# Kernel tuning notes

Hardware: AMD Instinct MI355X
Metric: run time of the kernel (lower is better)

The kernel has to match this reference:

```python
import jax, jax.numpy as jnp
import numpy as np

VOCAB = 50257
HIDDEN = 1024
CUTOFFS = [0, 20000, 40000, VOCAB]
N_CLUSTERS = 3
N_TOKENS = 4096


def setup_inputs() -> dict:
    key = jax.random.key(0)
    k1, k2, k3, k4 = jax.random.split(key, 4)
    x = jax.random.normal(k1, (N_TOKENS, HIDDEN), dtype=jnp.float32)
    y = jax.random.randint(k2, (N_TOKENS,), 0, VOCAB, dtype=jnp.int64)
    # nn.Linear(hidden, n_clusters, bias=False) weight: [n_clusters, hidden], init std=0.02
    W_cluster = jax.random.normal(k3, (N_CLUSTERS, HIDDEN), dtype=jnp.float32) * 0.02
    logits = jax.random.normal(k4, (HIDDEN, VOCAB), dtype=jnp.float32) * 0.02
    return {"x": x, "y": y, "W_cluster": W_cluster, "logits": logits}


def reference(x, y, W_cluster, logits):
    # cluster head: [N, n_clusters]
    cluster_ll = jax.nn.log_softmax(x @ W_cluster.T, axis=1)
    nll = jnp.zeros(y.shape, dtype=x.dtype)
    for i in range(N_CLUSTERS):  # small fixed loop over clusters
        l, r = CUTOFFS[i], CUTOFFS[i + 1]
        mask = (y >= l) & (y < r)
        # tail logits for this cluster's vocab slice: [N, r-l]
        tail_logprob = jax.nn.log_softmax(x @ logits[:, l:r], axis=1)
        t = jnp.clip(y - l, 0, r - l - 1)  # in-range for masked-out tokens
        tgt_lp = jnp.take_along_axis(tail_logprob, t[:, None], axis=1)[:, 0]
        val = -cluster_ll[:, i] - tgt_lp
        nll = jnp.where(mask, val, nll)
    return nll
```

## Files before the change

### kernel.cpp

```cpp
#include <hip/hip_runtime.h>
#include <math.h>

typedef unsigned short ushort_t;
typedef __attribute__((ext_vector_type(8))) short short8;
typedef __attribute__((ext_vector_type(4))) float floatx4;

constexpr int NT = 4096;
constexpr int H  = 1024;
constexpr int V  = 50257;
constexpr int CUT1 = 20000;
constexpr int CUT2 = 40000;

constexpr int NPAD_TOK = 4224;
constexpr int NPAD_COL = 50432;
constexpr int CT0 = 157, CT1 = 157, CT2 = 81;
constexpr int CT_TOTAL = CT0 + CT1 + CT2;
constexpr int MAX_TTILES = 32;
constexpr int CT_GROUPS = (CT_TOTAL + 7) / 8;
constexpr int MFMA_GRID = 8 * CT_GROUPS * MAX_TTILES;

constexpr int FB_TILES0 = (20000 + 63) / 64;
constexpr int FB_TILES1 = (20000 + 63) / 64;
constexpr int FB_TILES2 = (V - 40000 + 63) / 64;
constexpr int FB_TOTAL = FB_TILES0 + FB_TILES1 + FB_TILES2;

__device__ __forceinline__ ushort_t f2bf(float f) {
  unsigned int u = __float_as_uint(f);
  u = (u + 0x7FFFu + ((u >> 16) & 1u)) >> 16;
  return (ushort_t)u;
}
__device__ __forceinline__ float bf2f(ushort_t b) {
  return __uint_as_float(((unsigned int)b) << 16);
}
__device__ __forceinline__ void gl_lds16(const void* g, void* l) {
  __builtin_amdgcn_global_load_lds(
      (const __attribute__((address_space(1))) void*)g,
      (__attribute__((address_space(3))) void*)l, 16, 0, 0);
}

__global__ __launch_bounds__(1024) void setup_kernel(
    const int* __restrict__ y, int* __restrict__ offsets,
    int* __restrict__ perm, float* __restrict__ sumexp) {
  __shared__ int wcnt[16][3];
  __shared__ int wstart[16][3];
  int tid = threadIdx.x, lane = tid & 63, wid = tid >> 6;
  for (int i = tid; i < NT; i += 1024) sumexp[i] = 0.f;

  int kc[4];
  unsigned long long msk[4][3];
  int cw0 = 0, cw1 = 0, cw2 = 0;
  #pragma unroll
  for (int e = 0; e < 4; e++) {
    int v = y[tid + e * 1024];
    kc[e] = (v >= CUT1) + (v >= CUT2);
    msk[e][0] = __ballot(kc[e] == 0);
    msk[e][1] = __ballot(kc[e] == 1);
    msk[e][2] = __ballot(kc[e] == 2);
    cw0 += __popcll(msk[e][0]);
    cw1 += __popcll(msk[e][1]);
    cw2 += __popcll(msk[e][2]);
  }
  if (lane == 0) { wcnt[wid][0] = cw0; wcnt[wid][1] = cw1; wcnt[wid][2] = cw2; }
  __syncthreads();
  if (tid == 0) {
    int t0 = 0, t1 = 0, t2 = 0;
    for (int wv = 0; wv < 16; wv++) { t0 += wcnt[wv][0]; t1 += wcnt[wv][1]; t2 += wcnt[wv][2]; }
    offsets[0] = 0; offsets[1] = t0; offsets[2] = t0 + t1; offsets[3] = NT;
    int c0 = 0, c1 = t0, c2 = t0 + t1;
    for (int wv = 0; wv < 16; wv++) {
      wstart[wv][0] = c0; c0 += wcnt[wv][0];
      wstart[wv][1] = c1; c1 += wcnt[wv][1];
      wstart[wv][2] = c2; c2 += wcnt[wv][2];
    }
  }
  __syncthreads();
  int r0 = wstart[wid][0], r1 = wstart[wid][1], r2 = wstart[wid][2];
  unsigned long long below = (1ull << lane) - 1ull;
  #pragma unroll
  for (int e = 0; e < 4; e++) {
    int t = tid + e * 1024;
    int c = kc[e];
    int start = (c == 0) ? r0 : ((c == 1) ? r1 : r2);
    perm[start + __popcll(msk[e][c] & below)] = t;
    r0 += __popcll(msk[e][0]);
    r1 += __popcll(msk[e][1]);
    r2 += __popcll(msk[e][2]);
  }
}

__global__ __launch_bounds__(256) void gather_kernel(
    const float* __restrict__ x, const int* __restrict__ perm,
    ushort_t* __restrict__ xb) {
  int p = blockIdx.x;
  int src = (p < NT) ? perm[p] : -1;
  int k = threadIdx.x * 4;
  ushort4 o;
  if (src >= 0) {
    float4 v = *(const float4*)&x[(size_t)src * H + k];
    o.x = f2bf(v.x); o.y = f2bf(v.y); o.z = f2bf(v.z); o.w = f2bf(v.w);
  } else {
    o.x = 0; o.y = 0; o.z = 0; o.w = 0;
  }
  *(ushort4*)&xb[(size_t)p * H + k] = o;
}

__global__ __launch_bounds__(256) void transpose_kernel(
    const float* __restrict__ logits, ushort_t* __restrict__ lt) {
  __shared__ float ts[64][129];
  int col0 = blockIdx.x * 128, k0 = blockIdx.y * 64;
  int tid = threadIdx.x;
  #pragma unroll
  for (int e = 0; e < 8; e++) {
    int i = e * 256 + tid;
    int r = i >> 5, q = i & 31;
    int col = col0 + q * 4;
    float4 v;
    if (col + 3 < V) {
      v = *(const float4*)&logits[(size_t)(k0 + r) * V + col];
    } else {
      v.x = (col + 0 < V) ? logits[(size_t)(k0 + r) * V + col + 0] : 0.f;
      v.y = (col + 1 < V) ? logits[(size_t)(k0 + r) * V + col + 1] : 0.f;
      v.z = (col + 2 < V) ? logits[(size_t)(k0 + r) * V + col + 2] : 0.f;
      v.w = (col + 3 < V) ? logits[(size_t)(k0 + r) * V + col + 3] : 0.f;
    }
    ts[r][4 * q + 0] = v.x;
    ts[r][4 * q + 1] = v.y;
    ts[r][4 * q + 2] = v.z;
    ts[r][4 * q + 3] = v.w;
  }
  __syncthreads();
  #pragma unroll
  for (int e = 0; e < 4; e++) {
    int i = e * 256 + tid;
    int col = i >> 3, kq8 = i & 7;
    short8 o;
    #pragma unroll
    for (int d = 0; d < 8; d++) o[d] = (short)f2bf(ts[8 * kq8 + d][col]);
    *(short8*)&lt[(size_t)(col0 + col) * H + k0 + 8 * kq8] = o;
  }
}

__global__ __launch_bounds__(256) void head_kernel(
    const float* __restrict__ x, const int* __restrict__ y,
    const float* __restrict__ Wc, const ushort_t* __restrict__ lt,
    float* __restrict__ neg_cll, float* __restrict__ z_tgt) {
  int tid = threadIdx.x;
  int lane = tid & 63;
  int token = blockIdx.x * 4 + (tid >> 6);
  int yv = y[token];
  const float* xp = x + (size_t)token * H;
  const ushort_t* lp = lt + (size_t)yv * H;
  float c0 = 0.f, c1 = 0.f, c2 = 0.f, zt = 0.f;
  #pragma unroll
  for (int j = 0; j < 16; j++) {
    int h = lane + j * 64;
    float xv = xp[h];
    c0 = fmaf(xv, Wc[h], c0);
    c1 = fmaf(xv, Wc[H + h], c1);
    c2 = fmaf(xv, Wc[2 * H + h], c2);
    zt = fmaf(xv, bf2f(lp[h]), zt);
  }
  #pragma unroll
  for (int d = 32; d; d >>= 1) {
    c0 += __shfl_down(c0, d);
    c1 += __shfl_down(c1, d);
    c2 += __shfl_down(c2, d);
    zt += __shfl_down(zt, d);
  }
  if (lane == 0) {
    float m = fmaxf(c0, fmaxf(c1, c2));
    float lse = m + logf(expf(c0 - m) + expf(c1 - m) + expf(c2 - m));
    int k = (yv >= CUT1) + (yv >= CUT2);
    float ck = (k == 0) ? c0 : ((k == 1) ? c1 : c2);
    neg_cll[token] = lse - ck;
    z_tgt[token] = zt;
  }
}

__global__ __launch_bounds__(256) void mfma_kernel(
    const ushort_t* __restrict__ xb, const ushort_t* __restrict__ lt,
    const int* __restrict__ offsets, float* __restrict__ sumexp) {
  int id = blockIdx.x;
  int xcd = id & 7;
  int j = id >> 3;
  int ct = xcd + 8 * (j >> 5);
  int tt = j & 31;
  if (ct >= CT_TOTAL) return;

  int c, col0, colEnd;
  if (ct < CT0)            { c = 0; col0 = ct * 128;                      colEnd = CUT1; }
  else if (ct < CT0 + CT1) { c = 1; col0 = CUT1 + (ct - CT0) * 128;       colEnd = CUT2; }
  else                     { c = 2; col0 = CUT2 + (ct - CT0 - CT1) * 128; colEnd = V; }

  int t0 = offsets[c] + tt * 128;
  int tEnd = offsets[c + 1];
  if (t0 >= tEnd) return;

  __shared__ __align__(16) ushort_t xs[2][128 * 64];
  __shared__ __align__(16) ushort_t ls[2][128 * 64];

  int tid = threadIdx.x;
  int lane = tid & 63;
  int w = tid >> 6;
  int wm = w >> 1, wn = w & 1;
  int m_in = lane & 15, quad = lane >> 4;

  int srow = lane >> 3;
  int sc = lane & 7;
  int gchunk = sc ^ srow;
  const ushort_t* ga[4];
  const ushort_t* gb[4];
  int lofs[4];
  #pragma unroll
  for (int cc = 0; cc < 4; cc++) {
    int r0 = w * 32 + cc * 8;
    ga[cc] = xb + (size_t)(t0 + r0 + srow) * H + gchunk * 8;
    gb[cc] = lt + (size_t)(col0 + r0 + srow) * H + gchunk * 8;
    lofs[cc] = r0 * 64;
  }

  floatx4 acc[4][4];
  #pragma unroll
  for (int i = 0; i < 4; i++)
    #pragma unroll
    for (int jj = 0; jj < 4; jj++)
      acc[i][jj] = (floatx4){0.f, 0.f, 0.f, 0.f};

  auto STAGE = [&](int b) {
    #pragma unroll
    for (int cc = 0; cc < 4; cc++) {
      gl_lds16(ga[cc], &xs[b][lofs[cc]]);
      gl_lds16(gb[cc], &ls[b][lofs[cc]]);
      ga[cc] += 64; gb[cc] += 64;
    }
  };

  auto COMPUTE = [&](int b) {
    #pragma unroll
    for (int h = 0; h < 2; h++) {
      short8 af[4], bf[4];
      #pragma unroll
      for (int i = 0; i < 4; i++) {
        int row = wm * 64 + i * 16 + m_in;
        int slot = (h * 4 + quad) ^ (row & 7);
        af[i] = *(const short8*)&xs[b][row * 64 + slot * 8];
      }
      #pragma unroll
      for (int jj = 0; jj < 4; jj++) {
        int row = wn * 64 + jj * 16 + m_in;
        int slot = (h * 4 + quad) ^ (row & 7);
        bf[jj] = *(const short8*)&ls[b][row * 64 + slot * 8];
      }
      __builtin_amdgcn_s_setprio(1);
      #pragma unroll
      for (int i = 0; i < 4; i++)
        #pragma unroll
        for (int jj = 0; jj < 4; jj++)
          acc[i][jj] = __builtin_amdgcn_mfma_f32_16x16x32_bf16(af[i], bf[jj], acc[i][jj], 0, 0, 0);
      __builtin_amdgcn_s_setprio(0);
    }
  };

  STAGE(0);
  int cur = 0;
  #pragma unroll
  for (int t = 0; t < 15; ++t) {
    STAGE(cur ^ 1);
    asm volatile("s_waitcnt vmcnt(8)" ::: "memory");
    __builtin_amdgcn_sched_barrier(0);
    __builtin_amdgcn_s_barrier();
    __builtin_amdgcn_sched_barrier(0);
    COMPUTE(cur);
    __builtin_amdgcn_sched_barrier(0);
    __builtin_amdgcn_s_barrier();
    __builtin_amdgcn_sched_barrier(0);
    cur ^= 1;
  }
  asm volatile("s_waitcnt vmcnt(0)" ::: "memory");
  __builtin_amdgcn_sched_barrier(0);
  __builtin_amdgcn_s_barrier();
  __builtin_amdgcn_sched_barrier(0);
  COMPUTE(cur);

  __syncthreads();
  float* red = (float*)&xs[0][0];
  #pragma unroll
  for (int i = 0; i < 4; i++) {
    #pragma unroll
    for (int r = 0; r < 4; r++) {
      float s = 0.f;
      #pragma unroll
      for (int jj = 0; jj < 4; jj++) {
        int col = col0 + wn * 64 + jj * 16 + m_in;
        if (col < colEnd) s += __expf(acc[i][jj][r]);
      }
      s += __shfl_down(s, 8, 16);
      s += __shfl_down(s, 4, 16);
      s += __shfl_down(s, 2, 16);
      s += __shfl_down(s, 1, 16);
      if (m_in == 0) red[w * 64 + i * 16 + quad * 4 + r] = s;
    }
  }
  __syncthreads();
  if (tid < 128) {
    int rl = tid & 63, wm2 = tid >> 6;
    float s = red[(wm2 * 2 + 0) * 64 + rl] + red[(wm2 * 2 + 1) * 64 + rl];
    if (t0 + tid < tEnd) atomicAdd(&sumexp[t0 + tid], s);
  }
}

__global__ __launch_bounds__(256) void final_kernel(
    const int* __restrict__ perm, const float* __restrict__ neg_cll,
    const float* __restrict__ z_tgt, const float* __restrict__ sumexp,
    float* __restrict__ out) {
  int p = blockIdx.x * 256 + threadIdx.x;
  if (p < NT) {
    int t = perm[p];
    out[t] = neg_cll[t] + logf(sumexp[p]) - z_tgt[t];
  }
}

__global__ __launch_bounds__(256) void head_kernel_fb(
    const float* __restrict__ x, const int* __restrict__ y,
    const float* __restrict__ Wc, const float* __restrict__ logits,
    float* __restrict__ neg_cll, float* __restrict__ z_tgt) {
  int tid = threadIdx.x;
  int lane = tid & 63;
  int token = blockIdx.x * 4 + (tid >> 6);
  int yv = y[token];
  const float* xp = x + (size_t)token * H;
  float c0 = 0.f, c1 = 0.f, c2 = 0.f, zt = 0.f;
  #pragma unroll
  for (int j = 0; j < 16; j++) {
    int h = lane + j * 64;
    float xv = xp[h];
    c0 = fmaf(xv, Wc[h], c0);
    c1 = fmaf(xv, Wc[H + h], c1);
    c2 = fmaf(xv, Wc[2 * H + h], c2);
    zt = fmaf(xv, logits[(size_t)h * V + yv], zt);
  }
  #pragma unroll
  for (int d = 32; d; d >>= 1) {
    c0 += __shfl_down(c0, d);
    c1 += __shfl_down(c1, d);
    c2 += __shfl_down(c2, d);
    zt += __shfl_down(zt, d);
  }
  if (lane == 0) {
    float m = fmaxf(c0, fmaxf(c1, c2));
    float lse = m + logf(expf(c0 - m) + expf(c1 - m) + expf(c2 - m));
    int k = (yv >= CUT1) + (yv >= CUT2);
    float ck = (k == 0) ? c0 : ((k == 1) ? c1 : c2);
    neg_cll[token] = lse - ck;
    z_tgt[token] = zt;
  }
}

__global__ __launch_bounds__(256) void main_kernel_fb(
    const float* __restrict__ x, const float* __restrict__ logits,
    const int* __restrict__ offsets, const int* __restrict__ perm,
    float* __restrict__ sumexp) {
  int ct = blockIdx.x;
  int c, lct;
  if (ct < FB_TILES0)                  { c = 0; lct = ct; }
  else if (ct < FB_TILES0 + FB_TILES1) { c = 1; lct = ct - FB_TILES0; }
  else                                 { c = 2; lct = ct - FB_TILES0 - FB_TILES1; }
  int colBase = (c == 0) ? 0 : ((c == 1) ? CUT1 : CUT2);
  int colEnd  = (c == 0) ? CUT1 : ((c == 1) ? CUT2 : V);
  int col0 = colBase + lct * 64;
  int ncols = min(64, colEnd - col0);

  int t0 = offsets[c] + blockIdx.y * 64;
  int tEnd = offsets[c + 1];
  if (t0 >= tEnd) return;
  int ntok = min(64, tEnd - t0);

  __shared__ int tok_s[64];
  __shared__ float xsf[32][68];
  __shared__ float lsm[32][68];

  int tid = threadIdx.x;
  if (tid < 64) tok_s[tid] = perm[t0 + min(tid, ntok - 1)];
  __syncthreads();

  int tg = tid >> 4;
  int cg = tid & 15;
  float acc[4][4] = {};

  for (int h0 = 0; h0 < H; h0 += 32) {
    __syncthreads();
    #pragma unroll
    for (int e = 0; e < 8; e++) {
      int elem = e * 256 + tid;
      int tt = elem >> 5, kk = elem & 31;
      xsf[kk][tt] = x[(size_t)tok_s[tt] * H + h0 + kk];
    }
    #pragma unroll
    for (int e = 0; e < 8; e++) {
      int elem = e * 256 + tid;
      int kk = elem >> 6, cc = elem & 63;
      lsm[kk][cc] = (cc < ncols) ? logits[(size_t)(h0 + kk) * V + col0 + cc] : 0.f;
    }
    __syncthreads();
    #pragma unroll
    for (int kk = 0; kk < 32; kk++) {
      float4 xv = *(const float4*)&xsf[kk][4 * tg];
      float4 lv = *(const float4*)&lsm[kk][4 * cg];
      acc[0][0] = fmaf(xv.x, lv.x, acc[0][0]);
      acc[0][1] = fmaf(xv.x, lv.y, acc[0][1]);
      acc[0][2] = fmaf(xv.x, lv.z, acc[0][2]);
      acc[0][3] = fmaf(xv.x, lv.w, acc[0][3]);
      acc[1][0] = fmaf(xv.y, lv.x, acc[1][0]);
      acc[1][1] = fmaf(xv.y, lv.y, acc[1][1]);
      acc[1][2] = fmaf(xv.y, lv.z, acc[1][2]);
      acc[1][3] = fmaf(xv.y, lv.w, acc[1][3]);
      acc[2][0] = fmaf(xv.z, lv.x, acc[2][0]);
      acc[2][1] = fmaf(xv.z, lv.y, acc[2][1]);
      acc[2][2] = fmaf(xv.z, lv.z, acc[2][2]);
      acc[2][3] = fmaf(xv.z, lv.w, acc[2][3]);
      acc[3][0] = fmaf(xv.w, lv.x, acc[3][0]);
      acc[3][1] = fmaf(xv.w, lv.y, acc[3][1]);
      acc[3][2] = fmaf(xv.w, lv.z, acc[3][2]);
      acc[3][3] = fmaf(xv.w, lv.w, acc[3][3]);
    }
  }

  float s[4];
  #pragma unroll
  for (int i = 0; i < 4; i++) {
    float v = 0.f;
    #pragma unroll
    for (int j = 0; j < 4; j++) {
      if (4 * cg + j < ncols) v += expf(acc[i][j]);
    }
    s[i] = v;
  }
  #pragma unroll
  for (int i = 0; i < 4; i++) {
    #pragma unroll
    for (int d = 8; d; d >>= 1) s[i] += __shfl_down(s[i], d, 16);
  }
  if (cg == 0) {
    #pragma unroll
    for (int i = 0; i < 4; i++) {
      int tt = 4 * tg + i;
      if (tt < ntok) atomicAdd(&sumexp[tok_s[tt]], s[i]);
    }
  }
}

__global__ __launch_bounds__(256) void final_kernel_fb(
    const float* __restrict__ neg_cll, const float* __restrict__ z_tgt,
    const float* __restrict__ sumexp, float* __restrict__ out) {
  int i = blockIdx.x * 256 + threadIdx.x;
  if (i < NT) out[i] = neg_cll[i] + logf(sumexp[i]) - z_tgt[i];
}

extern "C" void kernel_launch(void* const* d_in, const int* in_sizes, int n_in,
                              void* d_out, int out_size, void* d_ws,
                              size_t ws_size, hipStream_t stream) {
  const float* x      = (const float*)d_in[0];
  const int*   y      = (const int*)d_in[1];
  const float* Wc     = (const float*)d_in[2];
  const float* logits = (const float*)d_in[3];
  float* out = (float*)d_out;

  char* ws = (char*)d_ws;
  int*   offsets = (int*)ws;
  int*   perm    = (int*)(ws + 256);
  float* sumexp  = (float*)(ws + 16896);
  float* neg_cll = (float*)(ws + 33280);
  float* z_tgt   = (float*)(ws + 49664);
  ushort_t* xb   = (ushort_t*)(ws + 66048);
  ushort_t* lt   = (ushort_t*)(ws + 66048 + (size_t)NPAD_TOK * H * 2);
  const size_t WS_NEED = 66048 + (size_t)NPAD_TOK * H * 2 + (size_t)NPAD_COL * H * 2;

  setup_kernel<<<1, 1024, 0, stream>>>(y, offsets, perm, sumexp);

  if (ws_size >= WS_NEED) {
    gather_kernel<<<NPAD_TOK, 256, 0, stream>>>(x, perm, xb);
    dim3 tg(NPAD_COL / 128, H / 64);
    transpose_kernel<<<tg, 256, 0, stream>>>(logits, lt);
    head_kernel<<<NT / 4, 256, 0, stream>>>(x, y, Wc, lt, neg_cll, z_tgt);
    mfma_kernel<<<MFMA_GRID, 256, 0, stream>>>(xb, lt, offsets, sumexp);
    final_kernel<<<NT / 256, 256, 0, stream>>>(perm, neg_cll, z_tgt, sumexp, out);
  } else {
    head_kernel_fb<<<NT / 4, 256, 0, stream>>>(x, y, Wc, logits, neg_cll, z_tgt);
    dim3 grid(FB_TOTAL, 64);
    main_kernel_fb<<<grid, 256, 0, stream>>>(x, logits, offsets, perm, sumexp);
    final_kernel_fb<<<NT / 256, 256, 0, stream>>>(neg_cll, z_tgt, sumexp, out);
  }
}
```

Before: 560.9 us.

## Enlarge MFMA GEMM tiles to 256x256 with 8 waves and 4-stage K pipeline

The fused GEMM+sumexp kernel moves from 128x128 output tiles with 4 waves and a 2-stage, K=64 double buffer to 256x256 tiles with 8 waves (each computing 128x64) and a 4-deep ring of K=32 slices with a new swizzled LDS layout. Larger tiles double the operand reuse per loaded byte and cut the number of global loads, atomics and blocks. A deeper prefetch hides latency with one barrier per K step. The cost is more register pressure (32 accumulators per wave), more padding waste on the cluster boundaries, and fewer blocks to fill the GPU.

Measured after the change: 582.8 us. 1.04x slower.

```diff
diff --git a/kernel.cpp b/kernel.cpp
--- a/kernel.cpp
+++ b/kernel.cpp
@@ -11,13 +11,14 @@
 constexpr int CUT1 = 20000;
 constexpr int CUT2 = 40000;
 
-constexpr int NPAD_TOK = 4224;
-constexpr int NPAD_COL = 50432;
-constexpr int CT0 = 157, CT1 = 157, CT2 = 81;
+constexpr int NPAD_TOK = 4352;
+constexpr int NPAD_COL = 50560;
+constexpr int CT0 = 79, CT1 = 79, CT2 = 41;
 constexpr int CT_TOTAL = CT0 + CT1 + CT2;
-constexpr int MAX_TTILES = 32;
+constexpr int MAX_TTILES = 16;
 constexpr int CT_GROUPS = (CT_TOTAL + 7) / 8;
 constexpr int MFMA_GRID = 8 * CT_GROUPS * MAX_TTILES;
+constexpr int NKT = H / 32;
 
 constexpr int FB_TILES0 = (20000 + 63) / 64;
 constexpr int FB_TILES1 = (20000 + 63) / 64;
@@ -177,115 +178,125 @@
   }
 }
 
-__global__ __launch_bounds__(256) void mfma_kernel(
+__global__ __launch_bounds__(512, 2) void mfma_kernel(
     const ushort_t* __restrict__ xb, const ushort_t* __restrict__ lt,
     const int* __restrict__ offsets, float* __restrict__ sumexp) {
   int id = blockIdx.x;
   int xcd = id & 7;
   int j = id >> 3;
-  int ct = xcd + 8 * (j >> 5);
-  int tt = j & 31;
+  int ct = xcd + 8 * (j >> 4);
+  int tt = j & 15;
   if (ct >= CT_TOTAL) return;
 
   int c, col0, colEnd;
-  if (ct < CT0)            { c = 0; col0 = ct * 128;                      colEnd = CUT1; }
-  else if (ct < CT0 + CT1) { c = 1; col0 = CUT1 + (ct - CT0) * 128;       colEnd = CUT2; }
-  else                     { c = 2; col0 = CUT2 + (ct - CT0 - CT1) * 128; colEnd = V; }
-
-  int t0 = offsets[c] + tt * 128;
+  if (ct < CT0)            { c = 0; col0 = ct * 256;                      colEnd = CUT1; }
+  else if (ct < CT0 + CT1) { c = 1; col0 = CUT1 + (ct - CT0) * 256;       colEnd = CUT2; }
+  else                     { c = 2; col0 = CUT2 + (ct - CT0 - CT1) * 256; colEnd = V; }
+
+  int t0 = offsets[c] + tt * 256;
   int tEnd = offsets[c + 1];
   if (t0 >= tEnd) return;
 
-  __shared__ __align__(16) ushort_t xs[2][128 * 64];
-  __shared__ __align__(16) ushort_t ls[2][128 * 64];
+  __shared__ __align__(16) ushort_t As[4][128 * 64];
+  __shared__ __align__(16) ushort_t Bs[4][128 * 64];
 
   int tid = threadIdx.x;
   int lane = tid & 63;
   int w = tid >> 6;
-  int wm = w >> 1, wn = w & 1;
+  int wm = w >> 2, wn = w & 3;
   int m_in = lane & 15, quad = lane >> 4;
 
-  int srow = lane >> 3;
-  int sc = lane & 7;
-  int gchunk = sc ^ srow;
-  const ushort_t* ga[4];
-  const ushort_t* gb[4];
-  int lofs[4];
-  #pragma unroll
-  for (int cc = 0; cc < 4; cc++) {
-    int r0 = w * 32 + cc * 8;
-    ga[cc] = xb + (size_t)(t0 + r0 + srow) * H + gchunk * 8;
-    gb[cc] = lt + (size_t)(col0 + r0 + srow) * H + gchunk * 8;
-    lofs[cc] = r0 * 64;
-  }
-
-  floatx4 acc[4][4];
-  #pragma unroll
-  for (int i = 0; i < 4; i++)
+  const ushort_t* gA[2];
+  const ushort_t* gB[2];
+  #pragma unroll
+  for (int cc = 0; cc < 2; cc++) {
+    int lr = w * 16 + cc * 8 + (lane >> 3);
+    int ls = lane & 7;
+    int m  = 2 * lr + (ls >> 2);
+    int q  = (ls & 3) ^ (lr & 3);
+    gA[cc] = xb + (size_t)(t0 + m) * H + q * 8;
+    gB[cc] = lt + (size_t)(col0 + m) * H + q * 8;
+  }
+  int ks = 0;
+  auto STAGE = [&]() {
+    int b = ks & 3;
+    #pragma unroll
+    for (int cc = 0; cc < 2; cc++) {
+      gl_lds16(gA[cc], &As[b][(w * 16 + cc * 8) * 64]);
+      gl_lds16(gB[cc], &Bs[b][(w * 16 + cc * 8) * 64]);
+      gA[cc] += 32; gB[cc] += 32;
+    }
+    ++ks;
+  };
+
+  int sxor = quad ^ ((m_in >> 1) & 3);
+  int aoff = (wm * 64 + (m_in >> 1)) * 64 + (m_in & 1) * 32 + sxor * 8;
+  int boff = (wn * 32 + (m_in >> 1)) * 64 + (m_in & 1) * 32 + sxor * 8;
+
+  floatx4 acc[8][4];
+  #pragma unroll
+  for (int i = 0; i < 8; i++)
     #pragma unroll
     for (int jj = 0; jj < 4; jj++)
       acc[i][jj] = (floatx4){0.f, 0.f, 0.f, 0.f};
 
-  auto STAGE = [&](int b) {
-    #pragma unroll
-    for (int cc = 0; cc < 4; cc++) {
-      gl_lds16(ga[cc], &xs[b][lofs[cc]]);
-      gl_lds16(gb[cc], &ls[b][lofs[cc]]);
-      ga[cc] += 64; gb[cc] += 64;
-    }
-  };
-
-  auto COMPUTE = [&](int b) {
-    #pragma unroll
-    for (int h = 0; h < 2; h++) {
-      short8 af[4], bf[4];
-      #pragma unroll
-      for (int i = 0; i < 4; i++) {
-        int row = wm * 64 + i * 16 + m_in;
-        int slot = (h * 4 + quad) ^ (row & 7);
-        af[i] = *(const short8*)&xs[b][row * 64 + slot * 8];
-      }
-      #pragma unroll
-      for (int jj = 0; jj < 4; jj++) {
-        int row = wn * 64 + jj * 16 + m_in;
-        int slot = (h * 4 + quad) ^ (row & 7);
-        bf[jj] = *(const short8*)&ls[b][row * 64 + slot * 8];
-      }
-      __builtin_amdgcn_s_setprio(1);
-      #pragma unroll
-      for (int i = 0; i < 4; i++)
-        #pragma unroll
-        for (int jj = 0; jj < 4; jj++)
-          acc[i][jj] = __builtin_amdgcn_mfma_f32_16x16x32_bf16(af[i], bf[jj], acc[i][jj], 0, 0, 0);
-      __builtin_amdgcn_s_setprio(0);
-    }
-  };
-
-  STAGE(0);
-  int cur = 0;
-  #pragma unroll
-  for (int t = 0; t < 15; ++t) {
-    STAGE(cur ^ 1);
-    asm volatile("s_waitcnt vmcnt(8)" ::: "memory");
-    __builtin_amdgcn_sched_barrier(0);
-    __builtin_amdgcn_s_barrier();
-    __builtin_amdgcn_sched_barrier(0);
-    COMPUTE(cur);
-    __builtin_amdgcn_sched_barrier(0);
-    __builtin_amdgcn_s_barrier();
-    __builtin_amdgcn_sched_barrier(0);
-    cur ^= 1;
-  }
-  asm volatile("s_waitcnt vmcnt(0)" ::: "memory");
+  STAGE(); STAGE(); STAGE();
+  asm volatile("s_waitcnt vmcnt(8)" ::: "memory");
   __builtin_amdgcn_sched_barrier(0);
   __builtin_amdgcn_s_barrier();
   __builtin_amdgcn_sched_barrier(0);
-  COMPUTE(cur);
-
-  __syncthreads();
-  float* red = (float*)&xs[0][0];
-  #pragma unroll
-  for (int i = 0; i < 4; i++) {
+
+  #pragma unroll 4
+  for (int k = 0; k < NKT; ++k) {
+    int b = k & 3;
+    const ushort_t* Ab = &As[b][0];
+    const ushort_t* Bb = &Bs[b][0];
+
+    if (k + 3 < NKT) STAGE();
+    __builtin_amdgcn_sched_barrier(0);
+
+    short8 af[4], bf[4];
+    #pragma unroll
+    for (int i = 0; i < 4; i++) af[i] = *(const short8*)&Ab[aoff + i * 512];
+    #pragma unroll
+    for (int jj = 0; jj < 4; jj++) bf[jj] = *(const short8*)&Bb[boff + jj * 512];
+
+    __builtin_amdgcn_s_setprio(1);
+    #pragma unroll
+    for (int i = 0; i < 4; i++)
+      #pragma unroll
+      for (int jj = 0; jj < 4; jj++)
+        acc[i][jj] = __builtin_amdgcn_mfma_f32_16x16x32_bf16(af[i], bf[jj], acc[i][jj], 0, 0, 0);
+    __builtin_amdgcn_s_setprio(0);
+
+    #pragma unroll
+    for (int i = 0; i < 4; i++) af[i] = *(const short8*)&Ab[aoff + (i + 4) * 512];
+
+    __builtin_amdgcn_s_setprio(1);
+    #pragma unroll
+    for (int i = 0; i < 4; i++)
+      #pragma unroll
+      for (int jj = 0; jj < 4; jj++)
+        acc[i + 4][jj] = __builtin_amdgcn_mfma_f32_16x16x32_bf16(af[i], bf[jj], acc[i + 4][jj], 0, 0, 0);
+    __builtin_amdgcn_s_setprio(0);
+
+    if (k < NKT - 1) {
+      if (k < NKT - 3) {
+        asm volatile("s_waitcnt vmcnt(8)" ::: "memory");
+      } else if (k == NKT - 3) {
+        asm volatile("s_waitcnt vmcnt(4)" ::: "memory");
+      } else {
+        asm volatile("s_waitcnt vmcnt(0)" ::: "memory");
+      }
+      __builtin_amdgcn_sched_barrier(0);
+      __builtin_amdgcn_s_barrier();
+      __builtin_amdgcn_sched_barrier(0);
+    }
+  }
+
+  float* red = (float*)&As[0][0];
+  #pragma unroll
+  for (int i = 0; i < 8; i++) {
     #pragma unroll
     for (int r = 0; r < 4; r++) {
       float s = 0.f;
@@ -298,14 +309,15 @@
       s += __shfl_down(s, 4, 16);
       s += __shfl_down(s, 2, 16);
       s += __shfl_down(s, 1, 16);
-      if (m_in == 0) red[w * 64 + i * 16 + quad * 4 + r] = s;
+      if (m_in == 0) red[w * 128 + i * 16 + quad * 4 + r] = s;
     }
   }
   __syncthreads();
-  if (tid < 128) {
-    int rl = tid & 63, wm2 = tid >> 6;
-    float s = red[(wm2 * 2 + 0) * 64 + rl] + red[(wm2 * 2 + 1) * 64 + rl];
-    if (t0 + tid < tEnd) atomicAdd(&sumexp[t0 + tid], s);
+  if (tid < 256) {
+    int row = tid, wm2 = row >> 7, rw = row & 127;
+    float s = red[(wm2 * 4 + 0) * 128 + rw] + red[(wm2 * 4 + 1) * 128 + rw] +
+              red[(wm2 * 4 + 2) * 128 + rw] + red[(wm2 * 4 + 3) * 128 + rw];
+    if (t0 + row < tEnd) atomicAdd(&sumexp[t0 + row], s);
   }
 }
 
@@ -482,7 +494,7 @@
     dim3 tg(NPAD_COL / 128, H / 64);
     transpose_kernel<<<tg, 256, 0, stream>>>(logits, lt);
     head_kernel<<<NT / 4, 256, 0, stream>>>(x, y, Wc, lt, neg_cll, z_tgt);
-    mfma_kernel<<<MFMA_GRID, 256, 0, stream>>>(xb, lt, offsets, sumexp);
+    mfma_kernel<<<MFMA_GRID, 512, 0, stream>>>(xb, lt, offsets, sumexp);
     final_kernel<<<NT / 256, 256, 0, stream>>>(perm, neg_cll, z_tgt, sumexp, out);
   } else {
     head_kernel_fb<<<NT / 4, 256, 0, stream>>>(x, y, Wc, logits, neg_cll, z_tgt);
```
